# Optimization experiments

Measured on AMD Instinct MI355X. Metric: run time of the kernel, lower is better.

The kernel has to match this reference:

```python
import jax, jax.numpy as jnp
import numpy as np

B, T, C, H = 4, 2048, 1024, 16
HD = C // H  # head dim = 64

def setup_inputs() -> dict:
    key = jax.random.key(0)
    k1, k2, k3 = jax.random.split(key, 3)
    x = jax.random.normal(k1, (B, T, C), dtype=jnp.float32)
    w_attn = jax.random.normal(k2, (C, 3 * C), dtype=jnp.float32) * 0.02
    w_proj = jax.random.normal(k3, (C, C), dtype=jnp.float32) * 0.02
    return {"x": x, "w_attn": w_attn, "w_proj": w_proj}

def reference(x, w_attn, w_proj):
    b, t, c = x.shape
    qkv = x @ w_attn  # [B,T,3C]
    q, k, v = jnp.split(qkv, 3, axis=-1)
    # [B,T,C] -> [B,H,T,HD]
    def heads(z):
        return z.reshape(b, t, H, HD).transpose(0, 2, 1, 3)
    q, k, v = heads(q), heads(k), heads(v)
    scale = 1.0 / jnp.sqrt(jnp.float32(HD))
    att = jnp.einsum('bhqd,bhkd->bhqk', q, k) * scale  # [B,H,T,T]
    causal = jnp.tril(jnp.ones((t, t), dtype=bool))
    att = jnp.where(causal[None, None], att, -jnp.inf)
    att = jax.nn.softmax(att, axis=-1)
    y = jnp.einsum('bhqk,bhkd->bhqd', att, v)  # [B,H,T,HD]
    y = y.transpose(0, 2, 1, 3).reshape(b, t, c)
    return y @ w_proj
```

## Files before the change

### kernel.cpp

```cpp
#include <hip/hip_runtime.h>
#include <hip/hip_bf16.h>

typedef short bf16x8 __attribute__((ext_vector_type(8)));
typedef short short4v __attribute__((ext_vector_type(4)));
typedef float f32x4 __attribute__((ext_vector_type(4)));

__device__ __forceinline__ short f2b(float f) {
  __hip_bfloat16 h = __float2bfloat16(f);
  union { __hip_bfloat16 h; short s; } u; u.h = h; return u.s;
}

__device__ __forceinline__ void async_copy16(const short* g, short* l) {
  __builtin_amdgcn_global_load_lds((const __attribute__((address_space(1))) void*)g,
                                   (__attribute__((address_space(3))) void*)l, 16, 0, 0);
}

__global__ __launch_bounds__(256) void cvt_kernel(const float* __restrict__ in,
                                                  short* __restrict__ out, int n4) {
  const int i = blockIdx.x * 256 + threadIdx.x;
  if (i >= n4) return;
  const float4 v = ((const float4*)in)[i];
  short4v o;
  o[0] = f2b(v.x); o[1] = f2b(v.y); o[2] = f2b(v.z); o[3] = f2b(v.w);
  ((short4v*)out)[i] = o;
}

__global__ __launch_bounds__(256) void tcvt_kernel(const float* __restrict__ in,
                                                   short* __restrict__ out, int R, int Cn,
                                                   int qscale_rows, float qscale) {
  __shared__ float t[32][33];
  const int tx = threadIdx.x, ty = threadIdx.y;
  const int c0 = blockIdx.x * 32, r0 = blockIdx.y * 32;
#pragma unroll
  for (int yy = 0; yy < 32; yy += 8)
    t[ty + yy][tx] = in[(size_t)(r0 + ty + yy) * Cn + (c0 + tx)];
  __syncthreads();
#pragma unroll
  for (int yy = 0; yy < 32; yy += 8) {
    const int orow = c0 + ty + yy;
    float v = t[tx][ty + yy];
    if (orow < qscale_rows) v *= qscale;
    out[(size_t)orow * R + (r0 + tx)] = f2b(v);
  }
}

__global__ __launch_bounds__(256) void vtrans_kernel(const short* __restrict__ qkv,
                                                     short* __restrict__ vT) {
  constexpr int T = 2048, C3 = 3072, HD = 64;
  const int bh = blockIdx.y, b = bh >> 4, h = bh & 15;
  const int t0 = blockIdx.x * 64;
  __shared__ short tile[64][72];
  const int tid = threadIdx.x;
  const int tr = tid >> 2, dc = (tid & 3) * 16;
  const short* src = qkv + (size_t)b * T * C3 + (size_t)(t0 + tr) * C3 + 2048 + h * HD + dc;
  *(bf16x8*)&tile[tr][dc] = *(const bf16x8*)src;
  *(bf16x8*)&tile[tr][dc + 8] = *(const bf16x8*)(src + 8);
  __syncthreads();
  const int dr = tid >> 2, tc = (tid & 3) * 16;
  bf16x8 o0, o1;
#pragma unroll
  for (int i = 0; i < 8; i++) o0[i] = tile[tc + i][dr];
#pragma unroll
  for (int i = 0; i < 8; i++) o1[i] = tile[tc + 8 + i][dr];
  short* dst = vT + ((size_t)bh * HD + dr) * T + t0 + tc;
  *(bf16x8*)dst = o0;
  *(bf16x8*)(dst + 8) = o1;
}

template <typename OutT>
__global__ __launch_bounds__(256) void gemm_bt_kernel(const short* __restrict__ A,
                                                      const short* __restrict__ Bt,
                                                      OutT* __restrict__ C,
                                                      int M, int N, int K) {
  __shared__ short As[128 * 32];
  __shared__ short Bs[128 * 32];
  const int tid = threadIdx.x;
  const int lane = tid & 63, wave = tid >> 6;
  const int quad = lane >> 4, l16 = lane & 15;

  const int nx = gridDim.x, ny = gridDim.y;
  const int nb = nx * ny, chunk = nb >> 3;
  const int flat = blockIdx.y * nx + blockIdx.x;
  const int nf = (flat & 7) * chunk + (flat >> 3);
  const int per_srow = 16 * nx;
  const int srw = nf / per_srow, idx = nf % per_srow;
  const int bm = srw * 16 + (idx & 15);
  const int bn = idx >> 4;
  const int m0 = bm * 128, n0 = bn * 128;
  const int wm = (wave >> 1) * 64, wn = (wave & 1) * 64;

  f32x4 acc[4][4] = {};

  const int lrow = wave * 32 + (lane >> 2);
  const int lcol = (lane & 3) * 8;
  const short* ga0 = A + (size_t)(m0 + lrow) * K + lcol;
  const short* ga1 = A + (size_t)(m0 + lrow + 16) * K + lcol;
  const short* gb0 = Bt + (size_t)(n0 + lrow) * K + lcol;
  const short* gb1 = Bt + (size_t)(n0 + lrow + 16) * K + lcol;
  short* la0 = &As[(wave * 2 + 0) * 512];
  short* la1 = &As[(wave * 2 + 1) * 512];
  short* lb0 = &Bs[(wave * 2 + 0) * 512];
  short* lb1 = &Bs[(wave * 2 + 1) * 512];

  for (int kt = 0; kt < K; kt += 32) {
    __syncthreads();
    async_copy16(ga0 + kt, la0);
    async_copy16(ga1 + kt, la1);
    async_copy16(gb0 + kt, lb0);
    async_copy16(gb1 + kt, lb1);
    __syncthreads();
    bf16x8 af[4], bfr[4];
#pragma unroll
    for (int mt = 0; mt < 4; mt++)
      af[mt] = *(const bf16x8*)&As[(wm + mt * 16 + l16) * 32 + quad * 8];
#pragma unroll
    for (int nt = 0; nt < 4; nt++)
      bfr[nt] = *(const bf16x8*)&Bs[(wn + nt * 16 + l16) * 32 + quad * 8];
#pragma unroll
    for (int mt = 0; mt < 4; mt++)
#pragma unroll
      for (int nt = 0; nt < 4; nt++)
        acc[mt][nt] = __builtin_amdgcn_mfma_f32_16x16x32_bf16(af[mt], bfr[nt], acc[mt][nt], 0, 0, 0);
  }

#pragma unroll
  for (int mt = 0; mt < 4; mt++)
#pragma unroll
    for (int nt = 0; nt < 4; nt++) {
      const int col = n0 + wn + nt * 16 + l16;
#pragma unroll
      for (int r = 0; r < 4; r++) {
        const int row = m0 + wm + mt * 16 + quad * 4 + r;
        const float v = acc[mt][nt][r];
        if constexpr (sizeof(OutT) == 4) {
          C[(size_t)row * N + col] = v;
        } else {
          C[(size_t)row * N + col] = f2b(v);
        }
      }
    }
}

__global__ __launch_bounds__(256, 2) void attn_kernel(const short* __restrict__ qkv,
                                                      const short* __restrict__ vT,
                                                      short* __restrict__ y) {
  constexpr int T = 2048, C3 = 3072, Cc = 1024, HD = 64;
  const int bh = blockIdx.y, b = bh >> 4, h = bh & 15;
  const int tid = threadIdx.x, lane = tid & 63, wave = tid >> 6;
  const int quad = lane >> 4, l16 = lane & 15;

  __shared__ short Ksb[2][64 * 64];
  __shared__ short Vtb[2][64 * 64];
  __shared__ short Ps[4][2][16 * 68];

  const size_t base = (size_t)b * T * C3;
  const int qcol = h * HD, kcol = Cc + h * HD;
  const size_t vtbase = (size_t)bh * HD * T;

  const int r8 = lane >> 3;
  const int cg8 = ((lane & 7) ^ r8) * 8;
  const short* gk[2];
  const short* gv[2];
  short* lk[2][2]; short* lv[2][2];
#pragma unroll
  for (int t8 = 0; t8 < 2; t8++) {
    const int row = wave * 16 + t8 * 8 + r8;
    gk[t8] = qkv + base + (size_t)row * C3 + kcol + cg8;
    gv[t8] = vT + vtbase + (size_t)row * T + cg8;
#pragma unroll
    for (int bu = 0; bu < 2; bu++) {
      lk[bu][t8] = &Ksb[bu][(wave * 16 + t8 * 8) * 64];
      lv[bu][t8] = &Vtb[bu][(wave * 16 + t8 * 8) * 64];
    }
  }
  const int sw0 = ((quad) ^ (l16 & 7)) * 8;
  const int sw1 = ((quad + 4) ^ (l16 & 7)) * 8;

  bf16x8 ones;
#pragma unroll
  for (int i = 0; i < 8; i++) ones[i] = (short)0x3F80;

  for (int half = 0; half < 2; half++) {
    const int t = half ? blockIdx.x : (15 - blockIdx.x);
    const int q0 = t * 128;
    const int jmax = 2 * t + 1;

    bf16x8 qf[2][2];
#pragma unroll
    for (int s = 0; s < 2; s++) {
      const short* qp = qkv + base + (size_t)(q0 + s * 64 + wave * 16 + l16) * C3 + qcol + quad * 8;
      qf[s][0] = *(const bf16x8*)qp;
      qf[s][1] = *(const bf16x8*)(qp + 32);
    }

    f32x4 o[2][4] = {};
    f32x4 l[2] = {};

    async_copy16(gk[0], lk[0][0]);
    async_copy16(gk[1], lk[0][1]);
    async_copy16(gv[0], lv[0][0]);
    async_copy16(gv[1], lv[0][1]);

    for (int j = 0; j <= jmax; j++) {
      const int cur = j & 1;
      __syncthreads();

      if (j < jmax) {
        const size_t ko = (size_t)(j + 1) * 64 * C3;
        const int vo = (j + 1) * 64;
        async_copy16(gk[0] + ko, lk[cur ^ 1][0]);
        async_copy16(gk[1] + ko, lk[cur ^ 1][1]);
        async_copy16(gv[0] + vo, lv[cur ^ 1][0]);
        async_copy16(gv[1] + vo, lv[cur ^ 1][1]);
      }

      bf16x8 kf[4][2], vf[4][2];
#pragma unroll
      for (int nt = 0; nt < 4; nt++) {
        const int rowb = (nt * 16 + l16) * 64;
        kf[nt][0] = *(const bf16x8*)&Ksb[cur][rowb + sw0];
        kf[nt][1] = *(const bf16x8*)&Ksb[cur][rowb + sw1];
        vf[nt][0] = *(const bf16x8*)&Vtb[cur][rowb + sw0];
        vf[nt][1] = *(const bf16x8*)&Vtb[cur][rowb + sw1];
      }

      const bool lo_act = (j < jmax);

#pragma unroll
      for (int s = 0; s < 2; s++) {
        if (s == 0 && !lo_act) continue;
        f32x4 sc[4];
#pragma unroll
        for (int nt = 0; nt < 4; nt++) {
          f32x4 a = {};
          a = __builtin_amdgcn_mfma_f32_16x16x32_bf16(qf[s][0], kf[nt][0], a, 0, 0, 0);
          a = __builtin_amdgcn_mfma_f32_16x16x32_bf16(qf[s][1], kf[nt][1], a, 0, 0, 0);
          sc[nt] = a;
        }
        const bool diag = (s == 0) ? (j == jmax - 1) : (j == jmax);
        if (diag) {
#pragma unroll
          for (int nt = 0; nt < 4; nt++)
#pragma unroll
            for (int r = 0; r < 4; r++) {
              const int row_l = wave * 16 + quad * 4 + r;
              const int col_l = nt * 16 + l16;
              if (col_l > row_l) sc[nt][r] = -INFINITY;
            }
        }
#pragma unroll
        for (int nt = 0; nt < 4; nt++)
#pragma unroll
          for (int r = 0; r < 4; r++)
            Ps[wave][s][(quad * 4 + r) * 68 + nt * 16 + l16] =
                f2b(__builtin_amdgcn_exp2f(sc[nt][r]));
      }
      asm volatile("s_waitcnt lgkmcnt(0)" ::: "memory");

#pragma unroll
      for (int s = 0; s < 2; s++) {
        if (s == 0 && !lo_act) continue;
        bf16x8 pa0 = *(const bf16x8*)&Ps[wave][s][l16 * 68 + quad * 8];
        bf16x8 pa1 = *(const bf16x8*)&Ps[wave][s][l16 * 68 + 32 + quad * 8];
        f32x4 lsum = {};
        lsum = __builtin_amdgcn_mfma_f32_16x16x32_bf16(pa0, ones, lsum, 0, 0, 0);
        lsum = __builtin_amdgcn_mfma_f32_16x16x32_bf16(pa1, ones, lsum, 0, 0, 0);
        l[s] += lsum;
#pragma unroll
        for (int nt = 0; nt < 4; nt++) {
          o[s][nt] = __builtin_amdgcn_mfma_f32_16x16x32_bf16(pa0, vf[nt][0], o[s][nt], 0, 0, 0);
          o[s][nt] = __builtin_amdgcn_mfma_f32_16x16x32_bf16(pa1, vf[nt][1], o[s][nt], 0, 0, 0);
        }
      }
    }

#pragma unroll
    for (int s = 0; s < 2; s++)
#pragma unroll
      for (int nt = 0; nt < 4; nt++)
#pragma unroll
        for (int r = 0; r < 4; r++) {
          const int row_g = q0 + s * 64 + wave * 16 + quad * 4 + r;
          y[(size_t)(b * T + row_g) * Cc + h * HD + nt * 16 + l16] = f2b(o[s][nt][r] / l[s][r]);
        }
  }
}

extern "C" void kernel_launch(void* const* d_in, const int* in_sizes, int n_in,
                              void* d_out, int out_size, void* d_ws, size_t ws_size,
                              hipStream_t stream) {
  constexpr int B = 4, T = 2048, C = 1024;
  constexpr int M = B * T;
  constexpr int N1 = 3 * C;
  const float* x      = (const float*)d_in[0];
  const float* w_attn = (const float*)d_in[1];
  const float* w_proj = (const float*)d_in[2];
  float* out = (float*)d_out;

  char* ws = (char*)d_ws;
  short* xb   = (short*)(ws + 0);
  short* waT  = (short*)(ws + 16777216);
  short* wpT  = (short*)(ws + 23068672);
  short* qkvb = (short*)(ws + 25165824);
  short* yb   = (short*)(ws + 75497472);
  short* vT   = xb;

  const float qscale = 0.125f * 1.44269504088896340736f;

  cvt_kernel<<<(M * C / 4 + 255) / 256, 256, 0, stream>>>(x, xb, M * C / 4);
  tcvt_kernel<<<dim3(N1 / 32, C / 32), dim3(32, 8), 0, stream>>>(w_attn, waT, C, N1, C, qscale);
  tcvt_kernel<<<dim3(C / 32, C / 32), dim3(32, 8), 0, stream>>>(w_proj, wpT, C, C, 0, 1.0f);
  gemm_bt_kernel<short><<<dim3(N1 / 128, M / 128), 256, 0, stream>>>(xb, waT, qkvb, M, N1, C);
  vtrans_kernel<<<dim3(T / 64, B * 16), 256, 0, stream>>>(qkvb, vT);
  attn_kernel<<<dim3(8, B * 16), 256, 0, stream>>>(qkvb, vT, yb);
  gemm_bt_kernel<float><<<dim3(C / 128, M / 128), 256, 0, stream>>>(yb, wpT, out, M, C, C);
}
```

Baseline: 271.6 us.

## Replace GEMMs with double-buffered 8-wave swizzled-LDS kernel and fuse preprocessing

Both projection GEMMs move to a new 512-thread kernel with 256-row tiles and K-step 64. It double-buffers LDS with asynchronous global-to-LDS loads issued in phases, uses an XOR swizzle to avoid bank conflicts, and raises wave priority around MFMA blocks. The aim is to overlap memory loads with matrix math and get more reuse per tile than the single-buffered 128x128 kernel. The three conversion/transpose launches are also merged into one kernel to cut launch overhead. The cost is more LDS and register pressure, and a hand-tuned vmcnt wait schedule that must match the order of issued loads.

Result: faster. 251.1 us (-7.5%).

```diff
diff --git a/kernel.cpp b/kernel.cpp
--- a/kernel.cpp
+++ b/kernel.cpp
@@ -5,6 +5,8 @@
 typedef short short4v __attribute__((ext_vector_type(4)));
 typedef float f32x4 __attribute__((ext_vector_type(4)));
 
+template <bool V> struct BoolC { static constexpr bool value = V; };
+
 __device__ __forceinline__ short f2b(float f) {
   __hip_bfloat16 h = __float2bfloat16(f);
   union { __hip_bfloat16 h; short s; } u; u.h = h; return u.s;
@@ -15,22 +17,28 @@
                                    (__attribute__((address_space(3))) void*)l, 16, 0, 0);
 }
 
-__global__ __launch_bounds__(256) void cvt_kernel(const float* __restrict__ in,
-                                                  short* __restrict__ out, int n4) {
-  const int i = blockIdx.x * 256 + threadIdx.x;
-  if (i >= n4) return;
-  const float4 v = ((const float4*)in)[i];
-  short4v o;
-  o[0] = f2b(v.x); o[1] = f2b(v.y); o[2] = f2b(v.z); o[3] = f2b(v.w);
-  ((short4v*)out)[i] = o;
-}
-
-__global__ __launch_bounds__(256) void tcvt_kernel(const float* __restrict__ in,
-                                                   short* __restrict__ out, int R, int Cn,
-                                                   int qscale_rows, float qscale) {
+__global__ __launch_bounds__(256) void pre_kernel(const float* __restrict__ x, short* __restrict__ xb,
+                                                  const float* __restrict__ wa, short* __restrict__ waT,
+                                                  const float* __restrict__ wp, short* __restrict__ wpT,
+                                                  float qscale) {
+  const int tid = threadIdx.x;
+  const int blk = blockIdx.x;
+  if (blk < 8192) {
+    const int i = blk * 256 + tid;
+    const float4 v = ((const float4*)x)[i];
+    short4v o;
+    o[0] = f2b(v.x); o[1] = f2b(v.y); o[2] = f2b(v.z); o[3] = f2b(v.w);
+    ((short4v*)xb)[i] = o;
+    return;
+  }
   __shared__ float t[32][33];
-  const int tx = threadIdx.x, ty = threadIdx.y;
-  const int c0 = blockIdx.x * 32, r0 = blockIdx.y * 32;
+  const float* in; short* out;
+  int idx, gxb, Cn, qrows; float qs;
+  if (blk < 11264) { idx = blk - 8192;  in = wa; out = waT; gxb = 96; Cn = 3072; qrows = 1024; qs = qscale; }
+  else             { idx = blk - 11264; in = wp; out = wpT; gxb = 32; Cn = 1024; qrows = 0;    qs = 1.0f; }
+  const int bx = idx % gxb, by = idx / gxb;
+  const int tx = tid & 31, ty = tid >> 5;
+  const int c0 = bx * 32, r0 = by * 32;
 #pragma unroll
   for (int yy = 0; yy < 32; yy += 8)
     t[ty + yy][tx] = in[(size_t)(r0 + ty + yy) * Cn + (c0 + tx)];
@@ -39,8 +47,8 @@
   for (int yy = 0; yy < 32; yy += 8) {
     const int orow = c0 + ty + yy;
     float v = t[tx][ty + yy];
-    if (orow < qscale_rows) v *= qscale;
-    out[(size_t)orow * R + (r0 + tx)] = f2b(v);
+    if (orow < qrows) v *= qs;
+    out[(size_t)orow * 1024 + (r0 + tx)] = f2b(v);
   }
 }
 
@@ -67,76 +75,111 @@
   *(bf16x8*)(dst + 8) = o1;
 }
 
-template <typename OutT>
-__global__ __launch_bounds__(256) void gemm_bt_kernel(const short* __restrict__ A,
-                                                      const short* __restrict__ Bt,
-                                                      OutT* __restrict__ C,
-                                                      int M, int N, int K) {
-  __shared__ short As[128 * 32];
-  __shared__ short Bs[128 * 32];
+template <int BN, typename OutT>
+__global__ __launch_bounds__(512, 2) void gemm8p_kernel(const short* __restrict__ A,
+                                                        const short* __restrict__ Bt,
+                                                        OutT* __restrict__ C,
+                                                        int M, int N, int K) {
+  constexpr int NB = BN / 64;
+  constexpr int NSTREAM = NB + 4;
+  __shared__ short ldsA[2][16384];
+  __shared__ short ldsB[2][NB * 4096];
+
   const int tid = threadIdx.x;
-  const int lane = tid & 63, wave = tid >> 6;
+  const int w = tid >> 6, lane = tid & 63;
   const int quad = lane >> 4, l16 = lane & 15;
-
-  const int nx = gridDim.x, ny = gridDim.y;
-  const int nb = nx * ny, chunk = nb >> 3;
-  const int flat = blockIdx.y * nx + blockIdx.x;
-  const int nf = (flat & 7) * chunk + (flat >> 3);
-  const int per_srow = 16 * nx;
-  const int srw = nf / per_srow, idx = nf % per_srow;
-  const int bm = srw * 16 + (idx & 15);
-  const int bn = idx >> 4;
-  const int m0 = bm * 128, n0 = bn * 128;
-  const int wm = (wave >> 1) * 64, wn = (wave & 1) * 64;
-
-  f32x4 acc[4][4] = {};
-
-  const int lrow = wave * 32 + (lane >> 2);
-  const int lcol = (lane & 3) * 8;
-  const short* ga0 = A + (size_t)(m0 + lrow) * K + lcol;
-  const short* ga1 = A + (size_t)(m0 + lrow + 16) * K + lcol;
-  const short* gb0 = Bt + (size_t)(n0 + lrow) * K + lcol;
-  const short* gb1 = Bt + (size_t)(n0 + lrow + 16) * K + lcol;
-  short* la0 = &As[(wave * 2 + 0) * 512];
-  short* la1 = &As[(wave * 2 + 1) * 512];
-  short* lb0 = &Bs[(wave * 2 + 0) * 512];
-  short* lb1 = &Bs[(wave * 2 + 1) * 512];
-
-  for (int kt = 0; kt < K; kt += 32) {
-    __syncthreads();
-    async_copy16(ga0 + kt, la0);
-    async_copy16(ga1 + kt, la1);
-    async_copy16(gb0 + kt, lb0);
-    async_copy16(gb1 + kt, lb1);
-    __syncthreads();
-    bf16x8 af[4], bfr[4];
-#pragma unroll
-    for (int mt = 0; mt < 4; mt++)
-      af[mt] = *(const bf16x8*)&As[(wm + mt * 16 + l16) * 32 + quad * 8];
-#pragma unroll
-    for (int nt = 0; nt < 4; nt++)
-      bfr[nt] = *(const bf16x8*)&Bs[(wn + nt * 16 + l16) * 32 + quad * 8];
-#pragma unroll
-    for (int mt = 0; mt < 4; mt++)
-#pragma unroll
-      for (int nt = 0; nt < 4; nt++)
-        acc[mt][nt] = __builtin_amdgcn_mfma_f32_16x16x32_bf16(af[mt], bfr[nt], acc[mt][nt], 0, 0, 0);
-  }
-
-#pragma unroll
-  for (int mt = 0; mt < 4; mt++)
-#pragma unroll
-    for (int nt = 0; nt < 4; nt++) {
-      const int col = n0 + wn + nt * 16 + l16;
-#pragma unroll
-      for (int r = 0; r < 4; r++) {
-        const int row = m0 + wm + mt * 16 + quad * 4 + r;
-        const float v = acc[mt][nt][r];
-        if constexpr (sizeof(OutT) == 4) {
-          C[(size_t)row * N + col] = v;
-        } else {
-          C[(size_t)row * N + col] = f2b(v);
-        }
+  const int half = w >> 2;
+  const int wn = (w & 3) * (BN / 4);
+  const int wm = half * 128;
+
+  const int gx = gridDim.x;
+  const int nwg = gx * gridDim.y;
+  const int flat = blockIdx.y * gx + blockIdx.x;
+  const int swz = (flat & 7) * (nwg >> 3) + (flat >> 3);
+  const int bn = swz % gx, bm = swz / gx;
+  const int m0 = bm * 256, n0 = bn * BN;
+
+  const int rsub = lane >> 3;
+  const int cl = (lane & 7) ^ rsub;
+  const short* pAsrc = A + (size_t)(m0 + half * 128 + (w & 3) * 8 + rsub) * K + cl * 8;
+  const short* pBsrc = Bt + (size_t)(n0 + w * 8 + rsub) * K + cl * 8;
+  const int dstoff = w * 512;
+
+  f32x4 acc[8][NB] = {};
+  bf16x8 bfr[NB][2];
+
+  auto issue = [&](int i, int buf, int tt) {
+    if (i < NB)
+      async_copy16(pBsrc + (size_t)(i * 64) * K + tt * 64, &ldsB[buf][i * 4096 + dstoff]);
+    else
+      async_copy16(pAsrc + (size_t)((i - NB) * 32) * K + tt * 64,
+                   &ldsA[buf][(i - NB) * 4096 + dstoff]);
+  };
+
+#pragma unroll
+  for (int i = 0; i < NSTREAM; ++i) issue(i, 0, 0);
+
+  const int NT = K >> 6;
+
+#define GEMM_PHASE(P, GS, GL)                                                                  \
+  {                                                                                            \
+    if constexpr (LAST) { asm volatile("s_waitcnt vmcnt(" #GL ")" ::: "memory"); }             \
+    else                { asm volatile("s_waitcnt vmcnt(" #GS ")" ::: "memory"); }             \
+    __builtin_amdgcn_s_barrier();                                                              \
+    asm volatile("" ::: "memory");                                                             \
+    bf16x8 af[2][2];                                                                           \
+    _Pragma("unroll") for (int mm = 0; mm < 2; ++mm)                                           \
+    _Pragma("unroll") for (int kh = 0; kh < 2; ++kh)                                           \
+      af[mm][kh] = *(const bf16x8*)&ldsA[buf][((P * 2 + half) * 32 + mm * 16 + l16) * 64 +     \
+                                              (((kh * 4 + quad) ^ (l16 & 7)) * 8)];            \
+    if constexpr (P == 0) {                                                                    \
+      _Pragma("unroll") for (int nf = 0; nf < NB; ++nf)                                        \
+      _Pragma("unroll") for (int kh = 0; kh < 2; ++kh)                                         \
+        bfr[nf][kh] = *(const bf16x8*)&ldsB[buf][(wn + nf * 16 + l16) * 64 +                   \
+                                                 (((kh * 4 + quad) ^ (l16 & 7)) * 8)];         \
+    }                                                                                          \
+    if constexpr (!LAST) {                                                                     \
+      if constexpr (2 * P < NSTREAM) issue(2 * P, buf ^ 1, t + 1);                             \
+      if constexpr (2 * P + 1 < NSTREAM) issue(2 * P + 1, buf ^ 1, t + 1);                     \
+    }                                                                                          \
+    __builtin_amdgcn_s_setprio(1);                                                             \
+    _Pragma("unroll") for (int mm = 0; mm < 2; ++mm)                                           \
+    _Pragma("unroll") for (int nf = 0; nf < NB; ++nf) {                                        \
+      acc[P * 2 + mm][nf] = __builtin_amdgcn_mfma_f32_16x16x32_bf16(af[mm][0], bfr[nf][0],     \
+                                                                    acc[P * 2 + mm][nf], 0, 0, 0); \
+      acc[P * 2 + mm][nf] = __builtin_amdgcn_mfma_f32_16x16x32_bf16(af[mm][1], bfr[nf][1],     \
+                                                                    acc[P * 2 + mm][nf], 0, 0, 0); \
+    }                                                                                          \
+    __builtin_amdgcn_s_setprio(0);                                                             \
+    __builtin_amdgcn_s_barrier();                                                              \
+  }
+
+  auto tile = [&](int t, auto lastc) {
+    constexpr bool LAST = decltype(lastc)::value;
+    const int buf = t & 1;
+    GEMM_PHASE(0, 3, 3)
+    GEMM_PHASE(1, 4, 2)
+    GEMM_PHASE(2, 5, 1)
+    GEMM_PHASE(3, 6, 0)
+  };
+
+  for (int t = 0; t < NT - 1; ++t) tile(t, BoolC<false>{});
+  tile(NT - 1, BoolC<true>{});
+#undef GEMM_PHASE
+
+  (void)M;
+#pragma unroll
+  for (int mf = 0; mf < 8; ++mf)
+#pragma unroll
+    for (int nf = 0; nf < NB; ++nf) {
+      const int col = n0 + wn + nf * 16 + l16;
+#pragma unroll
+      for (int r = 0; r < 4; ++r) {
+        const int row = m0 + wm + mf * 16 + quad * 4 + r;
+        if constexpr (sizeof(OutT) == 4)
+          C[(size_t)row * N + col] = acc[mf][nf][r];
+        else
+          C[(size_t)row * N + col] = f2b(acc[mf][nf][r]);
       }
     }
 }
@@ -307,11 +350,9 @@
 
   const float qscale = 0.125f * 1.44269504088896340736f;
 
-  cvt_kernel<<<(M * C / 4 + 255) / 256, 256, 0, stream>>>(x, xb, M * C / 4);
-  tcvt_kernel<<<dim3(N1 / 32, C / 32), dim3(32, 8), 0, stream>>>(w_attn, waT, C, N1, C, qscale);
-  tcvt_kernel<<<dim3(C / 32, C / 32), dim3(32, 8), 0, stream>>>(w_proj, wpT, C, C, 0, 1.0f);
-  gemm_bt_kernel<short><<<dim3(N1 / 128, M / 128), 256, 0, stream>>>(xb, waT, qkvb, M, N1, C);
+  pre_kernel<<<12288, 256, 0, stream>>>(x, xb, w_attn, waT, w_proj, wpT, qscale);
+  gemm8p_kernel<192, short><<<dim3(N1 / 192, M / 256), 512, 0, stream>>>(xb, waT, qkvb, M, N1, C);
   vtrans_kernel<<<dim3(T / 64, B * 16), 256, 0, stream>>>(qkvb, vT);
   attn_kernel<<<dim3(8, B * 16), 256, 0, stream>>>(qkvb, vT, yb);
-  gemm_bt_kernel<float><<<dim3(C / 128, M / 128), 256, 0, stream>>>(yb, wpT, out, M, C, C);
-}
+  gemm8p_kernel<128, float><<<dim3(C / 128, M / 256), 512, 0, stream>>>(yb, wpT, out, M, C, C);
+}
```
